# Kernel optimization log

Hardware: AMD Instinct MI355X
Metric: run time of the kernel (lower is better)

Reference implementation:

```python
import jax, jax.numpy as jnp
import numpy as np
import math

D = 1024
H = 16

def _new_gelu(x):
    return 0.5 * x * (1.0 + jnp.tanh(math.sqrt(2.0 / math.pi) * (x + 0.044715 * x ** 3)))

def _layer_norm(x, w):
    mu = jnp.mean(x, axis=-1, keepdims=True)
    var = jnp.var(x, axis=-1, keepdims=True)
    return (x - mu) * jax.lax.rsqrt(var + 1e-5) * w

def setup_inputs() -> dict:
    key = jax.random.key(0)
    ks = jax.random.split(key, 8)
    B, T = 2, 2048
    s = lambda fan_in: 1.0 / math.sqrt(fan_in)
    return {
        "x": jax.random.normal(ks[0], (B, T, D), jnp.float32),
        "ln1_w": jnp.ones((D,), jnp.float32),
        "attn_w": jax.random.normal(ks[1], (D, 3 * D), jnp.float32) * s(D),
        "attn_b": jnp.zeros((3 * D,), jnp.float32),
        "proj_w": jax.random.normal(ks[2], (D, D), jnp.float32) * s(D),
        "proj_b": jnp.zeros((D,), jnp.float32),
        "ln2_w": jnp.ones((D,), jnp.float32),
        "li1_w": jax.random.normal(ks[3], (D, 4 * D), jnp.float32) * s(D),
        "li1_b": jnp.zeros((4 * D,), jnp.float32),
        "li2_w": jax.random.normal(ks[4], (4 * D, D), jnp.float32) * s(4 * D),
        "li2_b": jnp.zeros((D,), jnp.float32),
    }

def reference(x, ln1_w, attn_w, attn_b, proj_w, proj_b, ln2_w, li1_w, li1_b, li2_w, li2_b):
    B, T, C = x.shape
    Dh = C // H
    # --- causal self-attention on pre-LN input ---
    h = _layer_norm(x, ln1_w)
    qkv = h @ attn_w + attn_b                      # [B,T,3C]
    q, k, v = jnp.split(qkv, 3, axis=-1)
    q = q.reshape(B, T, H, Dh)
    k = k.reshape(B, T, H, Dh)
    v = v.reshape(B, T, H, Dh)
    # NOTE: faithful to source — scale is 1/sqrt(BATCH), not 1/sqrt(head_dim)
    scale = 1.0 / math.sqrt(B)
    scores = jnp.einsum('bthd,bshd->bhts', q, k) * scale   # [B,H,T,T]
    causal = jnp.tril(jnp.ones((T, T), bool))
    scores = jnp.where(causal, scores, -jnp.inf)
    attn = jax.nn.softmax(scores, axis=-1)
    o = jnp.einsum('bhts,bshd->bthd', attn, v).reshape(B, T, C)
    x = x + o @ proj_w + proj_b
    # --- MLP ---
    h = _layer_norm(x, ln2_w)
    x = x + _new_gelu(h @ li1_w + li1_b) @ li2_w + li2_b
    return x
```

## Files before the change

kernel.cpp:

```cpp
#include <hip/hip_runtime.h>

typedef _Float16 f16;
typedef _Float16 f16x8 __attribute__((ext_vector_type(8)));
typedef _Float16 f16x4 __attribute__((ext_vector_type(4)));
typedef float    f32x4 __attribute__((ext_vector_type(4)));
typedef float    f32x16 __attribute__((ext_vector_type(16)));
typedef unsigned u32;
typedef unsigned u32x4 __attribute__((ext_vector_type(4)));

#define GAS __attribute__((address_space(1)))
#define LAS __attribute__((address_space(3)))

static __device__ __forceinline__ void gload_lds16(const void* g, void* l) {
    __builtin_amdgcn_global_load_lds((const GAS void*)g, (LAS void*)l, 16, 0, 0);
}

__global__ void wconv_t(const float* __restrict__ w, f16* __restrict__ wt, int K, int N) {
    __shared__ f16 t[32][33];
    const int tx = threadIdx.x, ty = threadIdx.y;
    const int n0 = blockIdx.x * 32, k0 = blockIdx.y * 32;
#pragma unroll
    for (int i = 0; i < 4; i++)
        t[ty + i * 8][tx] = (f16)w[(size_t)(k0 + ty + i * 8) * N + n0 + tx];
    __syncthreads();
#pragma unroll
    for (int i = 0; i < 4; i++)
        wt[(size_t)(n0 + ty + i * 8) * K + k0 + tx] = t[tx][ty + i * 8];
}

__global__ __launch_bounds__(256) void ln_kernel(const float* __restrict__ x,
                                                 const float* __restrict__ w,
                                                 f16* __restrict__ h) {
    const int row = blockIdx.x, tid = threadIdx.x;
    const float4 v = reinterpret_cast<const float4*>(x)[(size_t)row * 256 + tid];
    float s = v.x + v.y + v.z + v.w;
    float q = v.x * v.x + v.y * v.y + v.z * v.z + v.w * v.w;
#pragma unroll
    for (int m = 1; m < 64; m <<= 1) { s += __shfl_xor(s, m); q += __shfl_xor(q, m); }
    __shared__ float ss[4], qq[4];
    if ((tid & 63) == 0) { ss[tid >> 6] = s; qq[tid >> 6] = q; }
    __syncthreads();
    s = ss[0] + ss[1] + ss[2] + ss[3];
    q = qq[0] + qq[1] + qq[2] + qq[3];
    const float mu = s * (1.0f / 1024.0f);
    const float var = q * (1.0f / 1024.0f) - mu * mu;
    const float rs = rsqrtf(var + 1e-5f);
    const float4 wv = reinterpret_cast<const float4*>(w)[tid];
    f16x4 o;
    o[0] = (f16)((v.x - mu) * rs * wv.x);
    o[1] = (f16)((v.y - mu) * rs * wv.y);
    o[2] = (f16)((v.z - mu) * rs * wv.z);
    o[3] = (f16)((v.w - mu) * rs * wv.w);
    reinterpret_cast<f16x4*>(h)[(size_t)row * 256 + tid] = o;
}

__global__ __launch_bounds__(256) void vtrans(const f16* __restrict__ V, f16* __restrict__ Vt) {
    __shared__ f16 tl[64][72];
    const int tid = threadIdx.x;
    const int t0 = blockIdx.x * 64, bh = blockIdx.y;
    const int b = bh >> 4, hh = bh & 15;
    const int rr = tid >> 3, cc = (tid & 7) * 8;
#pragma unroll
    for (int p = 0; p < 2; p++) {
        f16x8 v = *(const f16x8*)(V + (size_t)(b * 2048 + t0 + p * 32 + rr) * 1024 + hh * 64 + cc);
#pragma unroll
        for (int j = 0; j < 8; j++) tl[p * 32 + rr][cc + j] = v[j];
    }
    __syncthreads();
#pragma unroll
    for (int p = 0; p < 2; p++) {
        const int d = p * 32 + rr;
        f16x8 o;
#pragma unroll
        for (int j = 0; j < 8; j++) o[j] = tl[cc + j][d];
        *(f16x8*)(Vt + (size_t)(bh * 64 + d) * 2048 + t0 + cc) = o;
    }
}

template <int EPI>
__global__ __launch_bounds__(512) void gemm_f16(
    const f16* __restrict__ A, int lda,
    const f16* __restrict__ Bt, int ldb,
    const float* __restrict__ bias,
    const float* __restrict__ res,
    void* __restrict__ outp,
    f16* __restrict__ oq, f16* __restrict__ ok, f16* __restrict__ ov,
    int N, int K) {
    __shared__ alignas(16) f16 As[3][128 * 32];
    __shared__ alignas(16) f16 Bs[3][128 * 32];
    const int tid = threadIdx.x;
    const int lane = tid & 63, wv = tid >> 6;
    const int wr = wv >> 2, wc = wv & 3;
    const int m0 = blockIdx.x * 128, n0 = blockIdx.y * 128;
    const int l15 = lane & 15, lg = lane >> 4;

    f32x4 acc[4][2] = {};

    const int ar = tid >> 2;
    const int ac = (tid & 3) * 8;
    const size_t koff = (size_t)blockIdx.z * K;
    const f16* gA = A + (size_t)(m0 + ar) * lda + ac + koff;
    const f16* gB = Bt + (size_t)(n0 + ar) * ldb + ac + koff;
    char* lA0 = (char*)As + wv * 1024;
    char* lB0 = (char*)Bs + wv * 1024;

    auto stage = [&](int buf, int k0) {
        gload_lds16(gA + k0, lA0 + buf * 8192);
        gload_lds16(gB + k0, lB0 + buf * 8192);
    };
    auto compute = [&](int buf) {
        f16x8 af[4], bf[2];
#pragma unroll
        for (int i = 0; i < 4; i++)
            af[i] = *(const f16x8*)&As[buf][(wr * 64 + i * 16 + l15) * 32 + lg * 8];
#pragma unroll
        for (int n = 0; n < 2; n++)
            bf[n] = *(const f16x8*)&Bs[buf][(wc * 32 + n * 16 + l15) * 32 + lg * 8];
#pragma unroll
        for (int mi = 0; mi < 4; mi++)
#pragma unroll
            for (int ni = 0; ni < 2; ni++)
                acc[mi][ni] = __builtin_amdgcn_mfma_f32_16x16x32_f16(af[mi], bf[ni], acc[mi][ni], 0, 0, 0);
    };

    const int nk = K >> 5;
    stage(0, 0);
    if (nk > 1) {
        stage(1, 32);
        asm volatile("s_waitcnt vmcnt(2)" ::: "memory");
    } else {
        asm volatile("s_waitcnt vmcnt(0)" ::: "memory");
    }
    __builtin_amdgcn_s_barrier();

    for (int t = 0; t < nk; ++t) {
        const bool pref = (t + 2 < nk);
        if (pref) stage((t + 2) % 3, (t + 2) * 32);
        compute(t % 3);
        if (t + 1 < nk) {
            if (pref) asm volatile("s_waitcnt vmcnt(2)" ::: "memory");
            else      asm volatile("s_waitcnt vmcnt(0)" ::: "memory");
            __builtin_amdgcn_s_barrier();
        }
    }

#pragma unroll
    for (int mi = 0; mi < 4; mi++) {
#pragma unroll
        for (int ni = 0; ni < 2; ni++) {
            const int gc = n0 + wc * 32 + ni * 16 + l15;
            const float bb = (EPI == 3) ? 0.0f : bias[gc];
#pragma unroll
            for (int r = 0; r < 4; r++) {
                const int gr = m0 + wr * 64 + mi * 16 + lg * 4 + r;
                float v = acc[mi][ni][r] + bb;
                if (EPI == 0) {
                    if (gc < 1024)      oq[(size_t)gr * 1024 + gc]        = (f16)(v * 0.70710678118654752f);
                    else if (gc < 2048) ok[(size_t)gr * 1024 + gc - 1024] = (f16)v;
                    else                ov[(size_t)gr * 1024 + gc - 2048] = (f16)v;
                } else if (EPI == 1) {
                    ((float*)outp)[(size_t)gr * N + gc] = v + res[(size_t)gr * N + gc];
                } else if (EPI == 2) {
                    const float z = 0.7978845608028654f * (v + 0.044715f * v * v * v);
                    const float t = 1.0f - 2.0f / (__builtin_amdgcn_exp2f(2.8853900817779268f * z) + 1.0f);
                    ((f16*)outp)[(size_t)gr * N + gc] = (f16)(0.5f * v * (1.0f + t));
                } else {
                    float* P = (float*)outp + (size_t)blockIdx.z * ((size_t)gridDim.x * 128) * N;
                    P[(size_t)gr * N + gc] = v;
                }
            }
        }
    }
}

__global__ __launch_bounds__(256) void kred(const float* __restrict__ p0,
                                            const float* __restrict__ p1,
                                            const float* __restrict__ bias,
                                            const float* __restrict__ res,
                                            float* __restrict__ out) {
    const size_t i = (size_t)blockIdx.x * 256 + threadIdx.x;
    const float4 a = ((const float4*)p0)[i];
    const float4 b = ((const float4*)p1)[i];
    const float4 r = ((const float4*)res)[i];
    const float4 w = ((const float4*)bias)[i & 255];
    float4 o;
    o.x = a.x + b.x + r.x + w.x;
    o.y = a.y + b.y + r.y + w.y;
    o.z = a.z + b.z + r.z + w.z;
    o.w = a.w + b.w + r.w + w.w;
    ((float4*)out)[i] = o;
}

__global__ __launch_bounds__(256) void attn_kernel(
    const f16* __restrict__ Q, const f16* __restrict__ Kb,
    const f16* __restrict__ Vt, f16* __restrict__ O) {
    __shared__ f16 ot[4][32][72];
    const int tid = threadIdx.x, lane = tid & 63, w = tid >> 6;
    const int l31 = lane & 31, hi = lane >> 5;
    const int bx = blockIdx.x;
    const int bh = bx & 31, j = bx >> 5;
    const int b = bh >> 4, hh = bh & 15;
    int qtile;
    if (w == 0) qtile = j;
    else if (w == 1) qtile = 31 - j;
    else if (w == 2) qtile = 32 + j;
    else qtile = 63 - j;
    const int q0 = qtile * 32;

    const f16* qrow = Q + (size_t)(b * 2048 + q0 + l31) * 1024 + hh * 64 + hi * 8;
    f16x8 qf[4];
#pragma unroll
    for (int s = 0; s < 4; s++) qf[s] = *(const f16x8*)(qrow + s * 16);

    f32x16 oacc[2] = {};
    float m = -3e38f, l = 0.0f;

    const f16* kbase = Kb + (size_t)b * 2048 * 1024 + hh * 64 + hi * 8;
    const f16* vrow0 = Vt + (size_t)(bh * 64 + l31) * 2048 + hi * 8;
    const f16* vrow1 = vrow0 + (size_t)32 * 2048;

    for (int kt = 0; kt <= qtile; ++kt) {
        const f16* kr = kbase + (size_t)(kt * 32 + l31) * 1024;
        f32x16 sacc = {};
#pragma unroll
        for (int s = 0; s < 4; s++) {
            const f16x8 kf = *(const f16x8*)(kr + s * 16);
            sacc = __builtin_amdgcn_mfma_f32_32x32x16_f16(kf, qf[s], sacc, 0, 0, 0);
        }
        f16x8 vf00 = *(const f16x8*)(vrow0 + kt * 32);
        f16x8 vf01 = *(const f16x8*)(vrow0 + kt * 32 + 16);
        f16x8 vf10 = *(const f16x8*)(vrow1 + kt * 32);
        f16x8 vf11 = *(const f16x8*)(vrow1 + kt * 32 + 16);

        if (kt == qtile) {
#pragma unroll
            for (int r = 0; r < 16; r++) {
                const int key = (r & 3) + 8 * (r >> 2) + 4 * hi;
                sacc[r] = (key > l31) ? -3e38f : sacc[r];
            }
        }
        float tm = sacc[0];
#pragma unroll
        for (int r = 1; r < 16; r++) tm = fmaxf(tm, sacc[r]);
        tm = fmaxf(tm, __shfl_xor(tm, 32));
        const float mnew = fmaxf(m, tm);
        const float alpha = __expf(m - mnew);
        m = mnew;
        float p[16], psum = 0.0f;
#pragma unroll
        for (int r = 0; r < 16; r++) { p[r] = __expf(sacc[r] - mnew); psum += p[r]; }
        psum += __shfl_xor(psum, 32);
        l = l * alpha + psum;

        u32 wd[8];
#pragma unroll
        for (int i = 0; i < 8; i++)
            wd[i] = __builtin_bit_cast(u32, __builtin_amdgcn_cvt_pkrtz(p[2 * i], p[2 * i + 1]));
        const u32 e0 = __shfl_xor(hi ? wd[0] : wd[2], 32);
        const u32 e1 = __shfl_xor(hi ? wd[1] : wd[3], 32);
        const u32 e2 = __shfl_xor(hi ? wd[4] : wd[6], 32);
        const u32 e3 = __shfl_xor(hi ? wd[5] : wd[7], 32);
        u32x4 b0, b1;
        b0[0] = hi ? e0 : wd[0]; b0[1] = hi ? e1 : wd[1];
        b0[2] = hi ? wd[2] : e0; b0[3] = hi ? wd[3] : e1;
        b1[0] = hi ? e2 : wd[4]; b1[1] = hi ? e3 : wd[5];
        b1[2] = hi ? wd[6] : e2; b1[3] = hi ? wd[7] : e3;
        const f16x8 pb0 = __builtin_bit_cast(f16x8, b0);
        const f16x8 pb1 = __builtin_bit_cast(f16x8, b1);

#pragma unroll
        for (int r = 0; r < 16; r++) { oacc[0][r] *= alpha; oacc[1][r] *= alpha; }
        oacc[0] = __builtin_amdgcn_mfma_f32_32x32x16_f16(vf00, pb0, oacc[0], 0, 0, 0);
        oacc[0] = __builtin_amdgcn_mfma_f32_32x32x16_f16(vf01, pb1, oacc[0], 0, 0, 0);
        oacc[1] = __builtin_amdgcn_mfma_f32_32x32x16_f16(vf10, pb0, oacc[1], 0, 0, 0);
        oacc[1] = __builtin_amdgcn_mfma_f32_32x32x16_f16(vf11, pb1, oacc[1], 0, 0, 0);
    }

    const float inv = 1.0f / l;
#pragma unroll
    for (int dt = 0; dt < 2; dt++)
#pragma unroll
        for (int r = 0; r < 16; r++) {
            const int d = dt * 32 + (r & 3) + 8 * (r >> 2) + 4 * hi;
            ot[w][l31][d] = (f16)(oacc[dt][r] * inv);
        }
    asm volatile("s_waitcnt lgkmcnt(0)" ::: "memory");
#pragma unroll
    for (int i = 0; i < 4; i++) {
        const int row = i * 8 + (lane >> 3), col = (lane & 7) * 8;
        const f16x8 o8 = *(const f16x8*)&ot[w][row][col];
        *(f16x8*)(O + (size_t)(b * 2048 + q0 + row) * 1024 + hh * 64 + col) = o8;
    }
}

extern "C" void kernel_launch(void* const* d_in, const int* in_sizes, int n_in,
                              void* d_out, int out_size, void* d_ws, size_t ws_size,
                              hipStream_t stream) {
    const float* x      = (const float*)d_in[0];
    const float* ln1_w  = (const float*)d_in[1];
    const float* attn_w = (const float*)d_in[2];
    const float* attn_b = (const float*)d_in[3];
    const float* proj_w = (const float*)d_in[4];
    const float* proj_b = (const float*)d_in[5];
    const float* ln2_w  = (const float*)d_in[6];
    const float* li1_w  = (const float*)d_in[7];
    const float* li1_b  = (const float*)d_in[8];
    const float* li2_w  = (const float*)d_in[9];
    const float* li2_b  = (const float*)d_in[10];
    float* out = (float*)d_out;

    char* ws = (char*)d_ws;
    size_t off = 0;
    auto alloc = [&](size_t bytes) { void* p = ws + off; off += (bytes + 255) & ~(size_t)255; return p; };
    f16* W1t = (f16*)alloc((size_t)3072 * 1024 * 2);
    f16* W2t = (f16*)alloc((size_t)1024 * 1024 * 2);
    f16* W3t = (f16*)alloc((size_t)4096 * 1024 * 2);
    f16* W4t = (f16*)alloc((size_t)1024 * 4096 * 2);
    f16* h   = (f16*)alloc((size_t)4096 * 1024 * 2);
    f16* Qb  = (f16*)alloc((size_t)4096 * 1024 * 2);
    f16* Kb  = (f16*)alloc((size_t)4096 * 1024 * 2);
    f16* Vb  = (f16*)alloc((size_t)4096 * 1024 * 2);
    f16* Vt  = (f16*)alloc((size_t)4096 * 1024 * 2);
    f16* Ob  = (f16*)alloc((size_t)4096 * 1024 * 2);
    float* x1 = (float*)alloc((size_t)4096 * 1024 * 4);
    float* P  = (float*)alloc((size_t)2 * 4096 * 1024 * 4);
    f16* Ab = Qb;

    dim3 b328(32, 8);
    wconv_t<<<dim3(96, 32),  b328, 0, stream>>>(attn_w, W1t, 1024, 3072);
    wconv_t<<<dim3(32, 32),  b328, 0, stream>>>(proj_w, W2t, 1024, 1024);
    wconv_t<<<dim3(128, 32), b328, 0, stream>>>(li1_w,  W3t, 1024, 4096);
    wconv_t<<<dim3(32, 128), b328, 0, stream>>>(li2_w,  W4t, 4096, 1024);

    ln_kernel<<<4096, 256, 0, stream>>>(x, ln1_w, h);
    gemm_f16<0><<<dim3(32, 24), 512, 0, stream>>>(h, 1024, W1t, 1024, attn_b, nullptr,
                                                  nullptr, Qb, Kb, Vb, 3072, 1024);
    vtrans<<<dim3(32, 32), 256, 0, stream>>>(Vb, Vt);
    attn_kernel<<<512, 256, 0, stream>>>(Qb, Kb, Vt, Ob);
    gemm_f16<1><<<dim3(32, 8), 512, 0, stream>>>(Ob, 1024, W2t, 1024, proj_b, x,
                                                 x1, nullptr, nullptr, nullptr, 1024, 1024);
    ln_kernel<<<4096, 256, 0, stream>>>(x1, ln2_w, h);
    gemm_f16<2><<<dim3(32, 32), 512, 0, stream>>>(h, 1024, W3t, 1024, li1_b, nullptr,
                                                  Ab, nullptr, nullptr, nullptr, 4096, 1024);
    gemm_f16<3><<<dim3(32, 8, 2), 512, 0, stream>>>(Ab, 4096, W4t, 4096, nullptr, nullptr,
                                                    P, nullptr, nullptr, nullptr, 1024, 2048);
    kred<<<4096, 256, 0, stream>>>(P, P + (size_t)4096 * 1024, li2_b, x1, out);
}
```

Before: 288.6 us.

## Software-pipeline K/V loads in attention and add lazy softmax rescaling

The attention loop now double-buffers K/V register fragments so the next tile's global loads are issued before the current tile's MFMAs. Each block now handles four consecutive query tiles, with the longest blocks dispatched first, replacing the old paired balancing. The online softmax only rescales when the running max grows by more than 8, uses exp2 with prescaled inputs and tree reductions, and raises wave priority around the MFMAs. Launch bounds request two blocks per SM. The extra registers may pressure occupancy, and the new tile mapping makes per-wave work within a block uneven.

Result: slower. 298.6 us (+3.5%).

```diff
diff --git a/kernel.cpp b/kernel.cpp
--- a/kernel.cpp
+++ b/kernel.cpp
@@ -191,20 +191,16 @@
     ((float4*)out)[i] = o;
 }
 
-__global__ __launch_bounds__(256) void attn_kernel(
+__global__ __launch_bounds__(256, 2) void attn_kernel(
     const f16* __restrict__ Q, const f16* __restrict__ Kb,
     const f16* __restrict__ Vt, f16* __restrict__ O) {
     __shared__ f16 ot[4][32][72];
     const int tid = threadIdx.x, lane = tid & 63, w = tid >> 6;
     const int l31 = lane & 31, hi = lane >> 5;
     const int bx = blockIdx.x;
-    const int bh = bx & 31, j = bx >> 5;
+    const int bh = bx & 31, jj = bx >> 5;
     const int b = bh >> 4, hh = bh & 15;
-    int qtile;
-    if (w == 0) qtile = j;
-    else if (w == 1) qtile = 31 - j;
-    else if (w == 2) qtile = 32 + j;
-    else qtile = 63 - j;
+    const int qtile = (15 - jj) * 4 + w;
     const int q0 = qtile * 32;
 
     const f16* qrow = Q + (size_t)(b * 2048 + q0 + l31) * 1024 + hh * 64 + hi * 8;
@@ -219,38 +215,62 @@
     const f16* vrow0 = Vt + (size_t)(bh * 64 + l31) * 2048 + hi * 8;
     const f16* vrow1 = vrow0 + (size_t)32 * 2048;
 
-    for (int kt = 0; kt <= qtile; ++kt) {
+    const int nt = qtile + 1;
+
+    f16x8 ka[4], va[4], kb2[4], vb2[4];
+    auto loadKV = [&](int kt, f16x8* kf, f16x8* vf) {
         const f16* kr = kbase + (size_t)(kt * 32 + l31) * 1024;
+#pragma unroll
+        for (int s = 0; s < 4; s++) kf[s] = *(const f16x8*)(kr + s * 16);
+        vf[0] = *(const f16x8*)(vrow0 + kt * 32);
+        vf[1] = *(const f16x8*)(vrow0 + kt * 32 + 16);
+        vf[2] = *(const f16x8*)(vrow1 + kt * 32);
+        vf[3] = *(const f16x8*)(vrow1 + kt * 32 + 16);
+    };
+
+    auto tilestep = [&](const f16x8* kf, const f16x8* vf, bool diag) {
         f32x16 sacc = {};
-#pragma unroll
-        for (int s = 0; s < 4; s++) {
-            const f16x8 kf = *(const f16x8*)(kr + s * 16);
-            sacc = __builtin_amdgcn_mfma_f32_32x32x16_f16(kf, qf[s], sacc, 0, 0, 0);
-        }
-        f16x8 vf00 = *(const f16x8*)(vrow0 + kt * 32);
-        f16x8 vf01 = *(const f16x8*)(vrow0 + kt * 32 + 16);
-        f16x8 vf10 = *(const f16x8*)(vrow1 + kt * 32);
-        f16x8 vf11 = *(const f16x8*)(vrow1 + kt * 32 + 16);
-
-        if (kt == qtile) {
+        __builtin_amdgcn_s_setprio(1);
+#pragma unroll
+        for (int s = 0; s < 4; s++)
+            sacc = __builtin_amdgcn_mfma_f32_32x32x16_f16(kf[s], qf[s], sacc, 0, 0, 0);
+        __builtin_amdgcn_s_setprio(0);
+        if (diag) {
 #pragma unroll
             for (int r = 0; r < 16; r++) {
                 const int key = (r & 3) + 8 * (r >> 2) + 4 * hi;
                 sacc[r] = (key > l31) ? -3e38f : sacc[r];
             }
         }
-        float tm = sacc[0];
-#pragma unroll
-        for (int r = 1; r < 16; r++) tm = fmaxf(tm, sacc[r]);
+        float t8[8];
+#pragma unroll
+        for (int i = 0; i < 8; i++) t8[i] = fmaxf(sacc[2 * i], sacc[2 * i + 1]);
+#pragma unroll
+        for (int i = 0; i < 4; i++) t8[i] = fmaxf(t8[i], t8[i + 4]);
+        float tm = fmaxf(fmaxf(t8[0], t8[1]), fmaxf(t8[2], t8[3]));
         tm = fmaxf(tm, __shfl_xor(tm, 32));
-        const float mnew = fmaxf(m, tm);
-        const float alpha = __expf(m - mnew);
-        m = mnew;
-        float p[16], psum = 0.0f;
-#pragma unroll
-        for (int r = 0; r < 16; r++) { p[r] = __expf(sacc[r] - mnew); psum += p[r]; }
+        const bool up = tm > m + 8.0f;
+        if (__any(up)) {
+            const float mnew = up ? tm : m;
+            const float alpha = __expf(m - mnew);
+            m = mnew;
+            l *= alpha;
+#pragma unroll
+            for (int r = 0; r < 16; r++) { oacc[0][r] *= alpha; oacc[1][r] *= alpha; }
+        }
+        const float mref = m * 1.44269504f;
+        float p[16];
+#pragma unroll
+        for (int r = 0; r < 16; r++)
+            p[r] = __builtin_amdgcn_exp2f(sacc[r] * 1.44269504f - mref);
+        float s8[8];
+#pragma unroll
+        for (int i = 0; i < 8; i++) s8[i] = p[2 * i] + p[2 * i + 1];
+#pragma unroll
+        for (int i = 0; i < 4; i++) s8[i] = s8[i] + s8[i + 4];
+        float psum = (s8[0] + s8[1]) + (s8[2] + s8[3]);
         psum += __shfl_xor(psum, 32);
-        l = l * alpha + psum;
+        l += psum;
 
         u32 wd[8];
 #pragma unroll
@@ -268,13 +288,23 @@
         const f16x8 pb0 = __builtin_bit_cast(f16x8, b0);
         const f16x8 pb1 = __builtin_bit_cast(f16x8, b1);
 
-#pragma unroll
-        for (int r = 0; r < 16; r++) { oacc[0][r] *= alpha; oacc[1][r] *= alpha; }
-        oacc[0] = __builtin_amdgcn_mfma_f32_32x32x16_f16(vf00, pb0, oacc[0], 0, 0, 0);
-        oacc[0] = __builtin_amdgcn_mfma_f32_32x32x16_f16(vf01, pb1, oacc[0], 0, 0, 0);
-        oacc[1] = __builtin_amdgcn_mfma_f32_32x32x16_f16(vf10, pb0, oacc[1], 0, 0, 0);
-        oacc[1] = __builtin_amdgcn_mfma_f32_32x32x16_f16(vf11, pb1, oacc[1], 0, 0, 0);
-    }
+        __builtin_amdgcn_s_setprio(1);
+        oacc[0] = __builtin_amdgcn_mfma_f32_32x32x16_f16(vf[0], pb0, oacc[0], 0, 0, 0);
+        oacc[0] = __builtin_amdgcn_mfma_f32_32x32x16_f16(vf[1], pb1, oacc[0], 0, 0, 0);
+        oacc[1] = __builtin_amdgcn_mfma_f32_32x32x16_f16(vf[2], pb0, oacc[1], 0, 0, 0);
+        oacc[1] = __builtin_amdgcn_mfma_f32_32x32x16_f16(vf[3], pb1, oacc[1], 0, 0, 0);
+        __builtin_amdgcn_s_setprio(0);
+    };
+
+    loadKV(0, ka, va);
+    int kt = 0;
+    for (; kt + 2 <= nt; kt += 2) {
+        loadKV(kt + 1, kb2, vb2);
+        tilestep(ka, va, false);
+        if (kt + 2 < nt) loadKV(kt + 2, ka, va);
+        tilestep(kb2, vb2, (kt + 1) == qtile);
+    }
+    if (kt < nt) tilestep(ka, va, true);
 
     const float inv = 1.0f / l;
 #pragma unroll
```
